# Performance work log

Measured on AMD Instinct MI355X. Metric: run time of the kernel, lower is better.

The kernel has to match this reference:

```python
import jax, jax.numpy as jnp
import numpy as np

B, DIM, NH, H, W_SP = 64, 768, 12, 56, 56
HEAD = DIM // NH
LAYER_DIM = 512
LN_EPS = 1e-5


def setup_inputs() -> dict:
    key = jax.random.key(0)
    k_x, k_q, k_w = jax.random.split(key, 3)
    x = jax.random.normal(k_x, (B, DIM, H, W_SP), dtype=jnp.float32)
    # trunc_normal_(std=1e-5) ~ tiny normal init for the learned query
    q = jax.random.normal(k_q, (1, NH, 1, HEAD), dtype=jnp.float32) * 1e-5
    Wl = jax.random.normal(k_w, (DIM, LAYER_DIM), dtype=jnp.float32) * (1.0 / np.sqrt(DIM))
    bl = jnp.zeros((LAYER_DIM,), dtype=jnp.float32)
    gamma = jnp.ones((LAYER_DIM,), dtype=jnp.float32)
    beta = jnp.zeros((LAYER_DIM,), dtype=jnp.float32)
    return {"x": x, "q": q, "Wl": Wl, "bl": bl, "gamma": gamma, "beta": beta}


def reference(x, q, Wl, bl, gamma, beta):
    b, d, h, w = x.shape
    nh, c = q.shape[1], q.shape[3]
    # 'b (nh c) h w -> b nh (h w) c'
    xr = x.reshape(b, nh, c, h * w).transpose(0, 1, 3, 2)  # [b, nh, hw, c]
    # single-query attention: scores [b, nh, 1, hw]
    attn = jnp.einsum('ahqc,bhnc->bhqn', q, xr)
    attn = jax.nn.softmax(attn, axis=-1)
    cls = jnp.einsum('bhqn,bhnc->bhqc', attn, xr)       # [b, nh, 1, c]
    cls = cls.transpose(0, 2, 1, 3).reshape(b, 1, nh * c)  # [b, 1, dim]
    # Linear + LayerNorm
    y = cls @ Wl + bl                                    # [b, 1, layer_dim]
    mu = jnp.mean(y, axis=-1, keepdims=True)
    var = jnp.mean((y - mu) ** 2, axis=-1, keepdims=True)
    y = (y - mu) * jax.lax.rsqrt(var + LN_EPS) * gamma + beta
    return y
```

## Files before the change

kernel.cpp:

```cpp
#include <hip/hip_runtime.h>
#include <hip/hip_bf16.h>
#include <math.h>

#define BATCH 64
#define DIM 768
#define NH 12
#define HEAD 64
#define NPOS 3136
#define LDIM 512
#define LN_EPS 1e-5f

__device__ float g_cls[BATCH * DIM];

__global__ __launch_bounds__(256, 2) void attn_pool_kernel(
    const float* __restrict__ x,
    const float* __restrict__ q,
    float* __restrict__ cls)
{
    const int bh = blockIdx.x;
    const int h  = bh % NH;
    const float* xp = x + (size_t)bh * HEAD * NPOS;
    const float* qp = q + h * HEAD;

    float qv[HEAD];
    #pragma unroll
    for (int c = 0; c < HEAD; ++c) qv[c] = qp[c];

    float o[HEAD];
    #pragma unroll
    for (int c = 0; c < HEAD; ++c) o[c] = 0.0f;
    float lsum = 0.0f;

    const int tid = threadIdx.x;

    for (int n = tid; n < NPOS; n += 256) {
        float xv[HEAD];
        #pragma unroll
        for (int c = 0; c < HEAD; ++c) xv[c] = xp[(size_t)c * NPOS + n];
        float s = 0.0f;
        #pragma unroll
        for (int c = 0; c < HEAD; ++c) s += qv[c] * xv[c];
        const float e = __expf(s);
        lsum += e;
        #pragma unroll
        for (int c = 0; c < HEAD; ++c) o[c] += e * xv[c];
    }

    const int lane = tid & 63;
    const int w    = tid >> 6;

    float rsum = 0.0f;
    #pragma unroll
    for (int c = 0; c < HEAD; ++c) {
        float v = o[c];
        v += __shfl_xor(v, 1);
        v += __shfl_xor(v, 2);
        v += __shfl_xor(v, 4);
        v += __shfl_xor(v, 8);
        v += __shfl_xor(v, 16);
        v += __shfl_xor(v, 32);
        if (lane == c) rsum = v;
    }
    float lv = lsum;
    lv += __shfl_xor(lv, 1);
    lv += __shfl_xor(lv, 2);
    lv += __shfl_xor(lv, 4);
    lv += __shfl_xor(lv, 8);
    lv += __shfl_xor(lv, 16);
    lv += __shfl_xor(lv, 32);

    __shared__ float sred[4][HEAD];
    __shared__ float slred[4];
    sred[w][lane] = rsum;
    if (lane == 0) slred[w] = lv;
    __syncthreads();

    if (tid < HEAD) {
        const float tot = sred[0][tid] + sred[1][tid] + sred[2][tid] + sred[3][tid];
        const float lt  = slred[0] + slred[1] + slred[2] + slred[3];
        cls[(size_t)bh * HEAD + tid] = tot / lt;
    }
}

__global__ __launch_bounds__(256) void linear_ln_kernel(
    const float* __restrict__ cls,
    const float* __restrict__ Wl,
    const float* __restrict__ bl,
    const float* __restrict__ gamma,
    const float* __restrict__ beta,
    float* __restrict__ out)
{
    const int b   = blockIdx.x;
    const int tid = threadIdx.x;
    const int j   = 2 * tid;

    __shared__ float cs[DIM];
    for (int k = tid; k < DIM; k += 256) cs[k] = cls[(size_t)b * DIM + k];
    __syncthreads();

    float2 a = *(const float2*)(bl + j);
    const float2* W2 = (const float2*)Wl;
    #pragma unroll 4
    for (int k = 0; k < DIM; ++k) {
        const float ck = cs[k];
        const float2 wv = W2[(size_t)k * (LDIM / 2) + tid];
        a.x += ck * wv.x;
        a.y += ck * wv.y;
    }

    const int lane = tid & 63;
    const int w    = tid >> 6;
    __shared__ float red1[4];
    __shared__ float red2[4];

    float v = a.x + a.y;
    v += __shfl_xor(v, 1);
    v += __shfl_xor(v, 2);
    v += __shfl_xor(v, 4);
    v += __shfl_xor(v, 8);
    v += __shfl_xor(v, 16);
    v += __shfl_xor(v, 32);
    if (lane == 0) red1[w] = v;
    __syncthreads();
    const float mu = (red1[0] + red1[1] + red1[2] + red1[3]) * (1.0f / LDIM);

    const float dx = a.x - mu;
    const float dy = a.y - mu;
    float v2 = dx * dx + dy * dy;
    v2 += __shfl_xor(v2, 1);
    v2 += __shfl_xor(v2, 2);
    v2 += __shfl_xor(v2, 4);
    v2 += __shfl_xor(v2, 8);
    v2 += __shfl_xor(v2, 16);
    v2 += __shfl_xor(v2, 32);
    if (lane == 0) red2[w] = v2;
    __syncthreads();
    const float var = (red2[0] + red2[1] + red2[2] + red2[3]) * (1.0f / LDIM);
    const float inv = rsqrtf(var + LN_EPS);

    const float2 g  = *(const float2*)(gamma + j);
    const float2 be = *(const float2*)(beta + j);
    float2 r;
    r.x = dx * inv * g.x + be.x;
    r.y = dy * inv * g.y + be.y;
    *(float2*)(out + (size_t)b * LDIM + j) = r;
}

extern "C" void kernel_launch(void* const* d_in, const int* in_sizes, int n_in,
                              void* d_out, int out_size, void* d_ws, size_t ws_size,
                              hipStream_t stream) {
    const float* x     = (const float*)d_in[0];
    const float* q     = (const float*)d_in[1];
    const float* Wl    = (const float*)d_in[2];
    const float* bl    = (const float*)d_in[3];
    const float* gamma = (const float*)d_in[4];
    const float* beta  = (const float*)d_in[5];
    float* out = (float*)d_out;

    float* cls;
    if (ws_size >= (size_t)BATCH * DIM * sizeof(float)) {
        cls = (float*)d_ws;
    } else {
        void* p = nullptr;
        (void)hipGetSymbolAddress(&p, HIP_SYMBOL(g_cls));
        cls = (float*)p;
    }

    attn_pool_kernel<<<BATCH * NH, 256, 0, stream>>>(x, q, cls);
    linear_ln_kernel<<<BATCH, 256, 0, stream>>>(cls, Wl, bl, gamma, beta, out);
}
```

Before: 869.4 us.

## Fuse attention pooling and linear+LayerNorm via last-block-per-batch atomic ticket

Measured after the change: 901.7 us. 3.7% more time.

```diff
diff --git a/kernel.cpp b/kernel.cpp
--- a/kernel.cpp
+++ b/kernel.cpp
@@ -1,5 +1,4 @@
 #include <hip/hip_runtime.h>
-#include <hip/hip_bf16.h>
 #include <math.h>
 
 #define BATCH 64
@@ -11,16 +10,24 @@
 #define LN_EPS 1e-5f
 
 __device__ float g_cls[BATCH * DIM];
+__device__ int   g_cnt[BATCH];
 
-__global__ __launch_bounds__(256, 2) void attn_pool_kernel(
+__global__ __launch_bounds__(256, 2) void decoder_fused_kernel(
     const float* __restrict__ x,
     const float* __restrict__ q,
-    float* __restrict__ cls)
+    const float* __restrict__ Wl,
+    const float* __restrict__ bl,
+    const float* __restrict__ gamma,
+    const float* __restrict__ beta,
+    float* __restrict__ out)
 {
     const int bh = blockIdx.x;
-    const int h  = bh % NH;
+    const int b  = bh / NH;
+    const int h  = bh - b * NH;
     const float* xp = x + (size_t)bh * HEAD * NPOS;
     const float* qp = q + h * HEAD;
+
+    const int tid = threadIdx.x;
 
     float qv[HEAD];
     #pragma unroll
@@ -30,8 +37,6 @@
     #pragma unroll
     for (int c = 0; c < HEAD; ++c) o[c] = 0.0f;
     float lsum = 0.0f;
-
-    const int tid = threadIdx.x;
 
     for (int n = tid; n < NPOS; n += 256) {
         float xv[HEAD];
@@ -78,24 +83,25 @@
     if (tid < HEAD) {
         const float tot = sred[0][tid] + sred[1][tid] + sred[2][tid] + sred[3][tid];
         const float lt  = slred[0] + slred[1] + slred[2] + slred[3];
-        cls[(size_t)bh * HEAD + tid] = tot / lt;
+        g_cls[(size_t)bh * HEAD + tid] = tot / lt;
     }
-}
 
-__global__ __launch_bounds__(256) void linear_ln_kernel(
-    const float* __restrict__ cls,
-    const float* __restrict__ Wl,
-    const float* __restrict__ bl,
-    const float* __restrict__ gamma,
-    const float* __restrict__ beta,
-    float* __restrict__ out)
-{
-    const int b   = blockIdx.x;
-    const int tid = threadIdx.x;
-    const int j   = 2 * tid;
+    __shared__ int sticket;
+    __syncthreads();
+    if (tid == 0) {
+        __threadfence();
+        sticket = __hip_atomic_fetch_add(&g_cnt[b], 1, __ATOMIC_ACQ_REL,
+                                         __HIP_MEMORY_SCOPE_AGENT);
+    }
+    __syncthreads();
+    if (sticket != NH - 1) return;
+
+    __threadfence();
+
+    const int j = 2 * tid;
 
     __shared__ float cs[DIM];
-    for (int k = tid; k < DIM; k += 256) cs[k] = cls[(size_t)b * DIM + k];
+    for (int k = tid; k < DIM; k += 256) cs[k] = g_cls[(size_t)b * DIM + k];
     __syncthreads();
 
     float2 a = *(const float2*)(bl + j);
@@ -108,8 +114,6 @@
         a.y += ck * wv.y;
     }
 
-    const int lane = tid & 63;
-    const int w    = tid >> 6;
     __shared__ float red1[4];
     __shared__ float red2[4];
 
@@ -144,6 +148,10 @@
     r.x = dx * inv * g.x + be.x;
     r.y = dy * inv * g.y + be.y;
     *(float2*)(out + (size_t)b * LDIM + j) = r;
+
+    if (tid == 0)
+        __hip_atomic_store(&g_cnt[b], 0, __ATOMIC_RELAXED,
+                           __HIP_MEMORY_SCOPE_AGENT);
 }
 
 extern "C" void kernel_launch(void* const* d_in, const int* in_sizes, int n_in,
@@ -157,15 +165,6 @@
     const float* beta  = (const float*)d_in[5];
     float* out = (float*)d_out;
 
-    float* cls;
-    if (ws_size >= (size_t)BATCH * DIM * sizeof(float)) {
-        cls = (float*)d_ws;
-    } else {
-        void* p = nullptr;
-        (void)hipGetSymbolAddress(&p, HIP_SYMBOL(g_cls));
-        cls = (float*)p;
-    }
-
-    attn_pool_kernel<<<BATCH * NH, 256, 0, stream>>>(x, q, cls);
-    linear_ln_kernel<<<BATCH, 256, 0, stream>>>(cls, Wl, bl, gamma, beta, out);
+    decoder_fused_kernel<<<BATCH * NH, 256, 0, stream>>>(
+        x, q, Wl, bl, gamma, beta, out);
 }
```
